# Optimization experiments

Hardware: AMD Instinct MI355X
Metric: run time of the kernel (lower is better)

Reference implementation:

```python
import jax, jax.numpy as jnp
import numpy as np
from jax import lax

T, L, K = 1024, 32, 128
BEG = 0  # index of '[BEG]' in the label dict


def setup_inputs() -> dict:
    key = jax.random.key(0)
    kx, kw, kl = jax.random.split(key, 3)
    X = jax.random.normal(kx, (T, L, L, K), dtype=jnp.float32)
    w = jax.random.normal(kw, (K,), dtype=jnp.float32)  # nn.Parameter, init N(0,1)
    label = jax.random.randint(kl, (T,), 0, L, dtype=jnp.int32)
    return {"X": X, "w": w, "label": label}


def reference(X, w, label):
    """CRF negative log-likelihood (forward algorithm over log-potential matrices)."""
    # Ms[t, i, j] = log-potential of transition i->j at step t  (X @ w)
    Ms = jnp.einsum('tijk,k->tij', X, w)  # [T, L, L]

    # forward recurrence: alpha_t[j] = logsumexp_i(alpha_{t-1}[i] + Ms[t, i, j])
    alpha0 = Ms[0, BEG, :]  # [L]

    def step(alpha, M):
        new = jax.nn.logsumexp(alpha[:, None] + M, axis=0)
        return new, None

    alpha_last, _ = lax.scan(step, alpha0, Ms[1:])
    logZ = jax.nn.logsumexp(alpha_last)

    # gold-path score: sum_t Ms[t, prev_label_t, label_t], prev_0 = BEG
    prev = jnp.concatenate([jnp.array([BEG], dtype=label.dtype), label[:-1]])
    t_idx = jnp.arange(Ms.shape[0])
    path_score = jnp.sum(Ms[t_idx, prev, label])

    return -path_score + logZ
```

## Files before the change

kernel.cpp:

```cpp
#include <hip/hip_runtime.h>

#define TT 1024
#define LL 32
#define KK 128
#define CHUNK 4
#define NBLK (TT/CHUNK)

#define ALPHA0_OFF 0
#define PATH_OFF   32
#define P0_OFF     288
#define P1_OFF     (P0_OFF + NBLK*1024)
#define P2_OFF     (P1_OFF + 64*1024)
#define P3_OFF     (P2_OFF + 16*1024)
#define P4_OFF     (P3_OFF + 4*1024)

__device__ __forceinline__ float lse_cell(const float A[LL][LL+1],
                                          const float B[LL][LL+1],
                                          int i, int j) {
  float s[LL];
  #pragma unroll
  for (int k = 0; k < LL; k++) s[k] = A[i][k] + B[k][j];
  float mx = s[0];
  #pragma unroll
  for (int k = 1; k < LL; k++) mx = fmaxf(mx, s[k]);
  float sum = 0.f;
  #pragma unroll
  for (int k = 0; k < LL; k++) sum += __expf(s[k] - mx);
  return mx + __logf(sum);
}

__global__ __launch_bounds__(1024, 1) void crf_stageA(
    const float4* __restrict__ X4, const float* __restrict__ w,
    const int* __restrict__ label, float* __restrict__ ws) {
  __shared__ float Ms[CHUNK][LL][LL + 1];
  __shared__ float Pb[2][LL][LL + 1];
  const int blk = blockIdx.x, tid = threadIdx.x;
  const int l5 = tid & 31;
  const int half = (tid >> 5) & 1;
  const int wid = tid >> 6;
  const int cellbase = wid * 2 + half;
  const float4 w4 = reinterpret_cast<const float4*>(w)[l5];
  const int t0 = blk * CHUNK;

  #pragma unroll
  for (int m = 0; m < CHUNK; m++) {
    #pragma unroll 4
    for (int it = 0; it < LL; it++) {
      const int cell = it * LL + cellbase;
      float4 xv = X4[(size_t)(t0 + m) * 1024u * 32u + (size_t)cell * 32u + l5];
      float v = xv.x * w4.x + xv.y * w4.y + xv.z * w4.z + xv.w * w4.w;
      v += __shfl_xor(v, 16, 32);
      v += __shfl_xor(v,  8, 32);
      v += __shfl_xor(v,  4, 32);
      v += __shfl_xor(v,  2, 32);
      v += __shfl_xor(v,  1, 32);
      if (l5 == 0) Ms[m][it][cellbase] = v;
    }
  }
  __syncthreads();

  if (tid == 0) {
    float ps = 0.f;
    for (int m = 0; m < CHUNK; m++) {
      const int t = t0 + m;
      const int lab = label[t];
      const int pv = (t == 0) ? 0 : label[t - 1];
      ps += Ms[m][pv][lab];
    }
    ws[PATH_OFF + blk] = ps;
  }
  if (blk == 0 && tid < LL) ws[ALPHA0_OFF + tid] = Ms[0][0][tid];

  const int i = tid >> 5, j = tid & 31;
  const int first = (blk == 0) ? 1 : 0;
  Pb[0][i][j] = lse_cell(Ms[first], Ms[first + 1], i, j);
  int cur = 0;
  for (int m = first + 2; m < CHUNK; m++) {
    __syncthreads();
    float r = lse_cell(Pb[cur], Ms[m], i, j);
    Pb[cur ^ 1][i][j] = r;
    cur ^= 1;
  }
  ws[P0_OFF + blk * 1024 + tid] = Pb[cur][i][j];
}

__global__ __launch_bounds__(1024, 1) void crf_combine(
    const float* __restrict__ src, float* __restrict__ dst, int radix) {
  __shared__ float A[2][LL][LL + 1];
  __shared__ float Bm[LL][LL + 1];
  const int blk = blockIdx.x, tid = threadIdx.x;
  const int i = tid >> 5, j = tid & 31;
  const float* sp = src + (size_t)blk * radix * 1024;
  A[0][i][j] = sp[tid];
  int cur = 0;
  for (int r = 1; r < radix; r++) {
    __syncthreads();
    Bm[i][j] = sp[(size_t)r * 1024 + tid];
    __syncthreads();
    float v = lse_cell(A[cur], Bm, i, j);
    A[cur ^ 1][i][j] = v;
    cur ^= 1;
  }
  dst[(size_t)blk * 1024 + tid] = A[cur][i][j];
}

__global__ __launch_bounds__(256, 1) void crf_final(
    const float* __restrict__ ws, float* __restrict__ out) {
  __shared__ float Pf[LL][LL + 1];
  __shared__ float a0[LL];
  __shared__ float al[LL];
  __shared__ float red[4];
  const int tid = threadIdx.x;
  for (int idx = tid; idx < 1024; idx += 256) Pf[idx >> 5][idx & 31] = ws[P4_OFF + idx];
  if (tid < LL) a0[tid] = ws[ALPHA0_OFF + tid];
  float ps = ws[PATH_OFF + tid];
  ps += __shfl_xor(ps, 32);
  ps += __shfl_xor(ps, 16);
  ps += __shfl_xor(ps,  8);
  ps += __shfl_xor(ps,  4);
  ps += __shfl_xor(ps,  2);
  ps += __shfl_xor(ps,  1);
  if ((tid & 63) == 0) red[tid >> 6] = ps;
  __syncthreads();
  if (tid < LL) {
    float s[LL];
    #pragma unroll
    for (int k = 0; k < LL; k++) s[k] = a0[k] + Pf[k][tid];
    float mx = s[0];
    #pragma unroll
    for (int k = 1; k < LL; k++) mx = fmaxf(mx, s[k]);
    float sum = 0.f;
    #pragma unroll
    for (int k = 0; k < LL; k++) sum += __expf(s[k] - mx);
    al[tid] = mx + __logf(sum);
  }
  __syncthreads();
  if (tid == 0) {
    float mx = al[0];
    for (int k = 1; k < LL; k++) mx = fmaxf(mx, al[k]);
    float sum = 0.f;
    for (int k = 0; k < LL; k++) sum += __expf(al[k] - mx);
    float logZ = mx + __logf(sum);
    float path = red[0] + red[1] + red[2] + red[3];
    out[0] = -path + logZ;
  }
}

extern "C" void kernel_launch(void* const* d_in, const int* in_sizes, int n_in,
                              void* d_out, int out_size, void* d_ws, size_t ws_size,
                              hipStream_t stream) {
  const float4* X4 = (const float4*)d_in[0];
  const float* w = (const float*)d_in[1];
  const int* label = (const int*)d_in[2];
  float* out = (float*)d_out;
  float* ws = (float*)d_ws;

  crf_stageA<<<NBLK, 1024, 0, stream>>>(X4, w, label, ws);
  crf_combine<<<64, 1024, 0, stream>>>(ws + P0_OFF, ws + P1_OFF, 4);
  crf_combine<<<16, 1024, 0, stream>>>(ws + P1_OFF, ws + P2_OFF, 4);
  crf_combine<<<4, 1024, 0, stream>>>(ws + P2_OFF, ws + P3_OFF, 4);
  crf_combine<<<1, 1024, 0, stream>>>(ws + P3_OFF, ws + P4_OFF, 4);
  crf_final<<<1, 256, 0, stream>>>(ws, out);
}
```

Measured before the change: 148.4 us.

## Collapse combine tree into radix-16 passes with register-resident log-semiring products

Replaces the four radix-4 combine launches plus the final kernel with one radix-16 combine pass and a fused radix-16 final kernel. Launch count drops from six to three. Each thread now keeps its row element in a register and broadcasts the A row via warp shuffles, so the shared-memory ping-pong buffer and one sync per step go away. The max reduction is tree-shaped and the exp sum uses eight accumulators to expose ILP. The stage A load loop is also flattened with wider unroll and FMA. The trade-off is longer serial chains per block: 15 dependent steps at low block counts instead of 3 steps across more levels.

```diff
diff --git a/kernel.cpp b/kernel.cpp
--- a/kernel.cpp
+++ b/kernel.cpp
@@ -2,7 +2,6 @@
 
 #define TT 1024
 #define LL 32
-#define KK 128
 #define CHUNK 4
 #define NBLK (TT/CHUNK)
 
@@ -10,57 +9,66 @@
 #define PATH_OFF   32
 #define P0_OFF     288
 #define P1_OFF     (P0_OFF + NBLK*1024)
-#define P2_OFF     (P1_OFF + 64*1024)
-#define P3_OFF     (P2_OFF + 16*1024)
-#define P4_OFF     (P3_OFF + 4*1024)
 
-__device__ __forceinline__ float lse_cell(const float A[LL][LL+1],
-                                          const float B[LL][LL+1],
-                                          int i, int j) {
+#define LDP (LL + 1)
+
+__device__ __forceinline__ float lse_mul_step(float a, const float* Bcol) {
   float s[LL];
   #pragma unroll
-  for (int k = 0; k < LL; k++) s[k] = A[i][k] + B[k][j];
-  float mx = s[0];
+  for (int k = 0; k < LL; k++) s[k] = __shfl(a, k, 32) + Bcol[k * LDP];
+  float t[LL];
   #pragma unroll
-  for (int k = 1; k < LL; k++) mx = fmaxf(mx, s[k]);
-  float sum = 0.f;
+  for (int k = 0; k < LL; k++) t[k] = s[k];
   #pragma unroll
-  for (int k = 0; k < LL; k++) sum += __expf(s[k] - mx);
+  for (int st = 16; st >= 1; st >>= 1) {
+    #pragma unroll
+    for (int k = 0; k < st; k++) t[k] = fmaxf(t[k], t[k + st]);
+  }
+  const float mx = t[0];
+  float a0 = 0.f, a1 = 0.f, a2 = 0.f, a3 = 0.f;
+  float a4 = 0.f, a5 = 0.f, a6 = 0.f, a7 = 0.f;
+  #pragma unroll
+  for (int k = 0; k < LL; k += 8) {
+    a0 += __expf(s[k]     - mx);
+    a1 += __expf(s[k + 1] - mx);
+    a2 += __expf(s[k + 2] - mx);
+    a3 += __expf(s[k + 3] - mx);
+    a4 += __expf(s[k + 4] - mx);
+    a5 += __expf(s[k + 5] - mx);
+    a6 += __expf(s[k + 6] - mx);
+    a7 += __expf(s[k + 7] - mx);
+  }
+  const float sum = ((a0 + a1) + (a2 + a3)) + ((a4 + a5) + (a6 + a7));
   return mx + __logf(sum);
 }
 
 __global__ __launch_bounds__(1024, 1) void crf_stageA(
     const float4* __restrict__ X4, const float* __restrict__ w,
     const int* __restrict__ label, float* __restrict__ ws) {
-  __shared__ float Ms[CHUNK][LL][LL + 1];
-  __shared__ float Pb[2][LL][LL + 1];
+  __shared__ float Ms[CHUNK][LL][LDP];
   const int blk = blockIdx.x, tid = threadIdx.x;
   const int l5 = tid & 31;
-  const int half = (tid >> 5) & 1;
-  const int wid = tid >> 6;
-  const int cellbase = wid * 2 + half;
+  const int grp = tid >> 5;
   const float4 w4 = reinterpret_cast<const float4*>(w)[l5];
-  const int t0 = blk * CHUNK;
+  const size_t base = (size_t)blk * CHUNK * 1024u * 32u;
 
-  #pragma unroll
-  for (int m = 0; m < CHUNK; m++) {
-    #pragma unroll 4
-    for (int it = 0; it < LL; it++) {
-      const int cell = it * LL + cellbase;
-      float4 xv = X4[(size_t)(t0 + m) * 1024u * 32u + (size_t)cell * 32u + l5];
-      float v = xv.x * w4.x + xv.y * w4.y + xv.z * w4.z + xv.w * w4.w;
-      v += __shfl_xor(v, 16, 32);
-      v += __shfl_xor(v,  8, 32);
-      v += __shfl_xor(v,  4, 32);
-      v += __shfl_xor(v,  2, 32);
-      v += __shfl_xor(v,  1, 32);
-      if (l5 == 0) Ms[m][it][cellbase] = v;
-    }
+  #pragma unroll 8
+  for (int q = 0; q < CHUNK * LL; q++) {
+    const int m = q >> 5, it = q & 31;
+    float4 xv = X4[base + (size_t)(m * 1024 + it * 32 + grp) * 32u + l5];
+    float v = fmaf(xv.x, w4.x, fmaf(xv.y, w4.y, fmaf(xv.z, w4.z, xv.w * w4.w)));
+    v += __shfl_xor(v, 16, 32);
+    v += __shfl_xor(v,  8, 32);
+    v += __shfl_xor(v,  4, 32);
+    v += __shfl_xor(v,  2, 32);
+    v += __shfl_xor(v,  1, 32);
+    if (l5 == 0) Ms[m][it][grp] = v;
   }
   __syncthreads();
 
   if (tid == 0) {
     float ps = 0.f;
+    const int t0 = blk * CHUNK;
     for (int m = 0; m < CHUNK; m++) {
       const int t = t0 + m;
       const int lab = label[t];
@@ -71,78 +79,65 @@
   }
   if (blk == 0 && tid < LL) ws[ALPHA0_OFF + tid] = Ms[0][0][tid];
 
-  const int i = tid >> 5, j = tid & 31;
+  const int i = grp, j = l5;
   const int first = (blk == 0) ? 1 : 0;
-  Pb[0][i][j] = lse_cell(Ms[first], Ms[first + 1], i, j);
-  int cur = 0;
-  for (int m = first + 2; m < CHUNK; m++) {
-    __syncthreads();
-    float r = lse_cell(Pb[cur], Ms[m], i, j);
-    Pb[cur ^ 1][i][j] = r;
-    cur ^= 1;
-  }
-  ws[P0_OFF + blk * 1024 + tid] = Pb[cur][i][j];
+  float a = Ms[first][i][j];
+  for (int m = first + 1; m < CHUNK; m++)
+    a = lse_mul_step(a, &Ms[m][0][j]);
+  ws[P0_OFF + blk * 1024 + tid] = a;
 }
 
-__global__ __launch_bounds__(1024, 1) void crf_combine(
-    const float* __restrict__ src, float* __restrict__ dst, int radix) {
-  __shared__ float A[2][LL][LL + 1];
-  __shared__ float Bm[LL][LL + 1];
+__global__ __launch_bounds__(1024, 1) void crf_combine16(
+    const float* __restrict__ src, float* __restrict__ dst) {
+  __shared__ float Bm[2][LL][LDP];
   const int blk = blockIdx.x, tid = threadIdx.x;
   const int i = tid >> 5, j = tid & 31;
-  const float* sp = src + (size_t)blk * radix * 1024;
-  A[0][i][j] = sp[tid];
-  int cur = 0;
-  for (int r = 1; r < radix; r++) {
+  const float* sp = src + (size_t)blk * 16 * 1024;
+  float a = sp[tid];
+  for (int r = 1; r < 16; r++) {
+    Bm[r & 1][i][j] = sp[r * 1024 + tid];
     __syncthreads();
-    Bm[i][j] = sp[(size_t)r * 1024 + tid];
-    __syncthreads();
-    float v = lse_cell(A[cur], Bm, i, j);
-    A[cur ^ 1][i][j] = v;
-    cur ^= 1;
+    a = lse_mul_step(a, &Bm[r & 1][0][j]);
   }
-  dst[(size_t)blk * 1024 + tid] = A[cur][i][j];
+  dst[(size_t)blk * 1024 + tid] = a;
 }
 
-__global__ __launch_bounds__(256, 1) void crf_final(
+__global__ __launch_bounds__(1024, 1) void crf_final16(
     const float* __restrict__ ws, float* __restrict__ out) {
-  __shared__ float Pf[LL][LL + 1];
-  __shared__ float a0[LL];
-  __shared__ float al[LL];
-  __shared__ float red[4];
+  __shared__ float Bm[2][LL][LDP];
+  __shared__ float redm[16], reds[16], redp[16];
   const int tid = threadIdx.x;
-  for (int idx = tid; idx < 1024; idx += 256) Pf[idx >> 5][idx & 31] = ws[P4_OFF + idx];
-  if (tid < LL) a0[tid] = ws[ALPHA0_OFF + tid];
-  float ps = ws[PATH_OFF + tid];
-  ps += __shfl_xor(ps, 32);
-  ps += __shfl_xor(ps, 16);
-  ps += __shfl_xor(ps,  8);
-  ps += __shfl_xor(ps,  4);
-  ps += __shfl_xor(ps,  2);
-  ps += __shfl_xor(ps,  1);
-  if ((tid & 63) == 0) red[tid >> 6] = ps;
+  const int i = tid >> 5, j = tid & 31;
+  const float* sp = ws + P1_OFF;
+  float a = sp[tid];
+  for (int r = 1; r < 16; r++) {
+    Bm[r & 1][i][j] = sp[r * 1024 + tid];
+    __syncthreads();
+    a = lse_mul_step(a, &Bm[r & 1][0][j]);
+  }
+  const float v = ws[ALPHA0_OFF + i] + a;
+  float m = v;
+  #pragma unroll
+  for (int o = 32; o >= 1; o >>= 1) m = fmaxf(m, __shfl_xor(m, o));
+  const int wid = tid >> 6, lane = tid & 63;
+  if (lane == 0) redm[wid] = m;
   __syncthreads();
-  if (tid < LL) {
-    float s[LL];
-    #pragma unroll
-    for (int k = 0; k < LL; k++) s[k] = a0[k] + Pf[k][tid];
-    float mx = s[0];
-    #pragma unroll
-    for (int k = 1; k < LL; k++) mx = fmaxf(mx, s[k]);
-    float sum = 0.f;
-    #pragma unroll
-    for (int k = 0; k < LL; k++) sum += __expf(s[k] - mx);
-    al[tid] = mx + __logf(sum);
+  float mb = redm[0];
+  #pragma unroll
+  for (int q = 1; q < 16; q++) mb = fmaxf(mb, redm[q]);
+  float e = __expf(v - mb);
+  float p = (tid < 256) ? ws[PATH_OFF + tid] : 0.f;
+  #pragma unroll
+  for (int o = 32; o >= 1; o >>= 1) {
+    e += __shfl_xor(e, o);
+    p += __shfl_xor(p, o);
   }
+  if (lane == 0) { reds[wid] = e; redp[wid] = p; }
   __syncthreads();
   if (tid == 0) {
-    float mx = al[0];
-    for (int k = 1; k < LL; k++) mx = fmaxf(mx, al[k]);
-    float sum = 0.f;
-    for (int k = 0; k < LL; k++) sum += __expf(al[k] - mx);
-    float logZ = mx + __logf(sum);
-    float path = red[0] + red[1] + red[2] + red[3];
-    out[0] = -path + logZ;
+    float s = 0.f, ps = 0.f;
+    for (int q = 0; q < 16; q++) { s += reds[q]; ps += redp[q]; }
+    out[0] = -ps + (mb + __logf(s));
   }
 }
 
@@ -156,9 +151,6 @@
   float* ws = (float*)d_ws;
 
   crf_stageA<<<NBLK, 1024, 0, stream>>>(X4, w, label, ws);
-  crf_combine<<<64, 1024, 0, stream>>>(ws + P0_OFF, ws + P1_OFF, 4);
-  crf_combine<<<16, 1024, 0, stream>>>(ws + P1_OFF, ws + P2_OFF, 4);
-  crf_combine<<<4, 1024, 0, stream>>>(ws + P2_OFF, ws + P3_OFF, 4);
-  crf_combine<<<1, 1024, 0, stream>>>(ws + P3_OFF, ws + P4_OFF, 4);
-  crf_final<<<1, 256, 0, stream>>>(ws, out);
+  crf_combine16<<<16, 1024, 0, stream>>>(ws + P0_OFF, ws + P1_OFF);
+  crf_final16<<<1, 1024, 0, stream>>>(ws, out);
 }
```

New measurement: 187.3 us. 1.26x slower.
